# Kernel tuning notes

Measured on AMD Instinct MI355X. Metric: run time of the kernel, lower is better.

The kernel has to match this reference:

```python
import jax, jax.numpy as jnp
import numpy as np

NPOINT = 1024
BRANCHES = [(0.4, 32), (0.8, 64)]  # (radius, nsample)
SPECS = [[67, 64, 64, 128], [67, 64, 128, 256]]  # mlp specs after use_xyz (+3)
EPS = 1e-5


def setup_inputs() -> dict:
    key = jax.random.key(0)
    ks = jax.random.split(key, 16)
    B, N, C = 8, 8192, 64
    inp = {
        "xyz": jax.random.normal(ks[0], (B, N, 3), jnp.float32),
        "features": jax.random.normal(ks[1], (B, C, N), jnp.float32),
    }
    ki = 2
    for bi, spec in enumerate(SPECS):
        for li in range(3):
            o, i = spec[li + 1], spec[li]
            inp[f"w{bi}_{li}"] = jax.random.normal(ks[ki], (o, i), jnp.float32) * (1.0 / np.sqrt(i)); ki += 1
            inp[f"g{bi}_{li}"] = jnp.ones((o,), jnp.float32)
            inp[f"b{bi}_{li}"] = jnp.zeros((o,), jnp.float32)
    return inp


def fps(pts, npoint):
    # pts: [B, N+1, 3] (mean point prepended); sequential farthest point sampling
    B, N1, _ = pts.shape

    def step(carry, _):
        dist, far = carry
        idx3 = jnp.broadcast_to(far[:, None, None], (B, 1, 3))
        centroid = jnp.take_along_axis(pts, idx3, axis=1)  # [B,1,3]
        d = jnp.sum((pts - centroid) ** 2, axis=-1)        # [B,N+1]
        dist = jnp.minimum(dist, d)
        far2 = jnp.argmax(dist, axis=-1)
        return (dist, far2), centroid[:, 0, :]

    dist0 = jnp.full((B, N1), 1e10, jnp.float32)
    far0 = jnp.zeros((B,), jnp.int32)
    _, locs = jax.lax.scan(step, (dist0, far0), None, length=npoint)
    return jnp.transpose(locs, (1, 0, 2))  # [B, npoint, 3]


def ball_query(xyz, new_xyz, radius, nsample):
    # first <=nsample indices with dist^2 < radius^2, padded with first valid (0 if none)
    B, N, _ = xyz.shape
    d2 = jnp.sum((new_xyz[:, :, None, :] - xyz[:, None, :, :]) ** 2, axis=-1)  # [B,S,N]
    score = jnp.where(d2 < radius * radius, jnp.arange(N, dtype=jnp.int32), N)
    vals, _ = jax.lax.top_k(-score, nsample)  # smallest scores = earliest valid indices
    idx = -vals                               # [B,S,nsample], N marks invalid
    first = idx[..., :1]
    first = jnp.where(first < N, first, 0)
    return jnp.where(idx < N, idx, first)


def _forward(xyz, features, params):
    mean = jnp.mean(xyz, axis=1, keepdims=True)
    pts = jnp.concatenate([mean, xyz], axis=1)          # prepend mean point
    new_xyz = jax.lax.stop_gradient(fps(pts, NPOINT))   # [B,npoint,3] (torch no_grad)
    outs = []
    for (radius, nsample), layers in zip(BRANCHES, params):
        idx = ball_query(xyz, new_xyz, radius, nsample)           # [B,S,K]
        gxyz = jax.vmap(lambda p, i: p[i])(xyz, idx)              # [B,S,K,3]
        rel = jnp.transpose(gxyz - new_xyz[:, :, None, :], (0, 3, 1, 2))  # [B,3,S,K]
        gfeat = jax.vmap(lambda f, i: f[:, i])(features, idx)     # [B,C,S,K]
        x = jnp.concatenate([rel, gfeat], axis=1)                 # [B,3+C,S,K]
        for W, g, b in layers:  # Conv2d 1x1 (no bias) + BatchNorm (train stats) + ReLU
            x = jnp.einsum('oi,bisk->bosk', W, x)
            m = jnp.mean(x, axis=(0, 2, 3), keepdims=True)
            v = jnp.var(x, axis=(0, 2, 3), keepdims=True)
            x = (x - m) / jnp.sqrt(v + EPS) * g[None, :, None, None] + b[None, :, None, None]
            x = jax.nn.relu(x)
        outs.append(jnp.max(x, axis=3))                           # [B,Cout,S]
    return new_xyz, jnp.concatenate(outs, axis=1)


def reference(xyz, features,
              w0_0, g0_0, b0_0, w0_1, g0_1, b0_1, w0_2, g0_2, b0_2,
              w1_0, g1_0, b1_0, w1_1, g1_1, b1_1, w1_2, g1_2, b1_2):
    params = [
        [(w0_0, g0_0, b0_0), (w0_1, g0_1, b0_1), (w0_2, g0_2, b0_2)],
        [(w1_0, g1_0, b1_0), (w1_1, g1_1, b1_1), (w1_2, g1_2, b1_2)],
    ]
    return _forward(xyz, features, params)
```

## Files before the change

kernel.cpp:

```cpp
#include <hip/hip_runtime.h>
#include <hip/hip_bf16.h>
#include <cstdint>


typedef __attribute__((ext_vector_type(8))) short short8;
typedef __attribute__((ext_vector_type(4))) float f32x4;

__device__ __forceinline__ float bf2f(unsigned short u) {
    return __uint_as_float(((unsigned)u) << 16);
}
__device__ __forceinline__ unsigned short f2bf(float f) {
    unsigned u = __float_as_uint(f);
    return (unsigned short)((u + 0x7fffu + ((u >> 16) & 1u)) >> 16);
}

__device__ __forceinline__ float wave_red_max_f32(float v) {
#define DPPSTEP(ctrl)                                                                  \
    {                                                                                  \
        int _t = __builtin_amdgcn_update_dpp((int)0xFF800000, __float_as_int(v), ctrl, \
                                             0xf, 0xf, false);                         \
        v = fmaxf(v, __int_as_float(_t));                                              \
    }
    DPPSTEP(0x111) DPPSTEP(0x112) DPPSTEP(0x114) DPPSTEP(0x118) DPPSTEP(0x142) DPPSTEP(0x143)
#undef DPPSTEP
    return v;
}
__device__ __forceinline__ unsigned wave_red_min_u32(unsigned v) {
#define DPPSTEP(ctrl)                                                                   \
    {                                                                                   \
        unsigned _t = (unsigned)__builtin_amdgcn_update_dpp((int)0xFFFFFFFF, (int)v,    \
                                                            ctrl, 0xf, 0xf, false);     \
        v = v < _t ? v : _t;                                                            \
    }
    DPPSTEP(0x111) DPPSTEP(0x112) DPPSTEP(0x114) DPPSTEP(0x118) DPPSTEP(0x142) DPPSTEP(0x143)
#undef DPPSTEP
    return v;
}

static const size_t OFF_WBF   = 0;
static const size_t OFF_STATS = 262144;
static const size_t STATS_BYTES = 720896;
static const size_t OFF_AFF   = 1048576;
static const size_t OFF_IDX0  = 2097152;
static const size_t OFF_IDX1  = 3145728;
static const size_t OFF_MX    = 5242880;
static const size_t OFF_MN    = 13631488;
static const size_t OFF_Y0    = 22020096;
static const size_t OFF_Y1    = 90177536;
static const size_t OFF_FEATT = 211812352;

__global__ void prep_wbf(const float* __restrict__ w0, const float* __restrict__ w1,
                         const float* __restrict__ w2, const float* __restrict__ w3,
                         const float* __restrict__ w4, const float* __restrict__ w5,
                         unsigned short* __restrict__ wb) {
    int id = blockIdx.x * 256 + threadIdx.x;
    const int psz[6] = {6144, 4096, 8192, 6144, 8192, 32768};
    const int Kp[6] = {96, 64, 64, 96, 64, 128};
    const int Ks[6] = {67, 64, 64, 67, 64, 128};
    const float* wp[6] = {w0, w1, w2, w3, w4, w5};
    int off = 0;
    for (int l = 0; l < 6; ++l) {
        if (id < off + psz[l]) {
            int e = id - off;
            int m = e / Kp[l], k = e - m * Kp[l];
            float v = (k < Ks[l]) ? wp[l][m * Ks[l] + k] : 0.f;
            wb[id] = f2bf(v);
            return;
        }
        off += psz[l];
    }
}

__global__ __launch_bounds__(256) void feat_transpose(const float* __restrict__ xyz,
                                                      const float* __restrict__ feat,
                                                      unsigned short* __restrict__ ft) {
    __shared__ float tile[64][65];
    const int b = blockIdx.y;
    const int j0 = blockIdx.x * 64;
    const int tid = threadIdx.x;
#pragma unroll
    for (int i = 0; i < 16; ++i) {
        int e = i * 256 + tid;
        int c = e >> 6, j = e & 63;
        tile[j][c] = feat[((size_t)b * 64 + c) * 8192 + j0 + j];
    }
    __syncthreads();
#pragma unroll
    for (int i = 0; i < 16; ++i) {
        int e = i * 256 + tid;
        int j = e >> 6, c = e & 63;
        ft[((size_t)(b * 8192 + j0 + j)) * 96 + 3 + c] = f2bf(tile[j][c]);
    }
    if (tid < 64) {
        int j = tid;
        size_t base = ((size_t)(b * 8192 + j0 + j)) * 96;
        const float* xp = xyz + ((size_t)b * 8192 + j0 + j) * 3;
        ft[base + 0] = f2bf(xp[0]);
        ft[base + 1] = f2bf(xp[1]);
        ft[base + 2] = f2bf(xp[2]);
    } else if (tid < 128) {
        int j = tid - 64;
        size_t base = ((size_t)(b * 8192 + j0 + j)) * 96;
        for (int c = 67; c < 96; ++c) ft[base + c] = 0;
    }
}

__global__ __launch_bounds__(512) void fps_kernel(const float* __restrict__ xyz,
                                                  float* __restrict__ newxyz) {
    const int b = blockIdx.x;
    const int t = threadIdx.x;
    const int lane = t & 63, wv = t >> 6;
    const float* xb = xyz + (size_t)b * 8192 * 3;

    __shared__ float ptsx[8200];
    __shared__ float ptsy[8200];
    __shared__ float ptsz[8200];
    __shared__ float ldsM[16][3];
    __shared__ float meanv[3];
    __shared__ alignas(16) unsigned long long sKey[2][8];

    float px[16], py[16], pz[16], d[16];
#pragma unroll
    for (int j = 0; j < 16; ++j) {
        int q = t + 512 * j;
        px[j] = xb[q * 3 + 0];
        py[j] = xb[q * 3 + 1];
        pz[j] = xb[q * 3 + 2];
        d[j] = 1e10f;
        ptsx[q + 1] = px[j];
        ptsy[q + 1] = py[j];
        ptsz[q + 1] = pz[j];
    }
    float sxA = 0.f, syA = 0.f, szA = 0.f;
    float sxB = 0.f, syB = 0.f, szB = 0.f;
    int uA = (t + 1023) & 1023;
    int uB = (t + 511) & 1023;
#pragma unroll
    for (int j = 0; j < 8; ++j) {
        int ia = uA + 1024 * j;
        int ib = uB + 1024 * j;
        sxA += xb[ia * 3 + 0]; syA += xb[ia * 3 + 1]; szA += xb[ia * 3 + 2];
        sxB += xb[ib * 3 + 0]; syB += xb[ib * 3 + 1]; szB += xb[ib * 3 + 2];
    }
#pragma unroll
    for (int off = 32; off; off >>= 1) {
        sxA += __shfl_xor(sxA, off, 64);
        syA += __shfl_xor(syA, off, 64);
        szA += __shfl_xor(szA, off, 64);
        sxB += __shfl_xor(sxB, off, 64);
        syB += __shfl_xor(syB, off, 64);
        szB += __shfl_xor(szB, off, 64);
    }
    if (lane == 0) {
        ldsM[wv][0] = sxA; ldsM[wv][1] = syA; ldsM[wv][2] = szA;
        ldsM[wv + 8][0] = sxB; ldsM[wv + 8][1] = syB; ldsM[wv + 8][2] = szB;
    }
    __syncthreads();
    if (t < 3) {
        float s = 0.f;
        for (int w = 0; w < 16; ++w) s += ldsM[w][t];
        meanv[t] = s * (1.f / 8192.f);
    }
    __syncthreads();
    float cx = meanv[0], cy = meanv[1], cz = meanv[2];
    const float mmx = cx, mmy = cy, mmz = cz;
    float dm = 1e10f;
    if (t == 0) { ptsx[0] = cx; ptsy[0] = cy; ptsz[0] = cz; }
    __syncthreads();

    for (int it = 0; it < 1024; ++it) {
        if (t == 0) {
            float* o = newxyz + ((size_t)b * 1024 + it) * 3;
            o[0] = cx; o[1] = cy; o[2] = cz;
        }
        float vmax = -1e30f;
#pragma unroll
        for (int j = 0; j < 16; ++j) {
            float dx = __fsub_rn(px[j], cx);
            float dy = __fsub_rn(py[j], cy);
            float dz = __fsub_rn(pz[j], cz);
            float dd = __fadd_rn(__fadd_rn(__fmul_rn(dx, dx), __fmul_rn(dy, dy)), __fmul_rn(dz, dz));
            float nd = fminf(d[j], dd);
            d[j] = nd;
            vmax = fmaxf(vmax, nd);
        }
        if (t == 0) {
            float dx = __fsub_rn(mmx, cx);
            float dy = __fsub_rn(mmy, cy);
            float dz = __fsub_rn(mmz, cz);
            float dd = __fadd_rn(__fadd_rn(__fmul_rn(dx, dx), __fmul_rn(dy, dy)), __fmul_rn(dz, dz));
            dm = fminf(dm, dd);
            vmax = fmaxf(vmax, dm);
        }
        float wm = wave_red_max_f32(vmax);
        float bmaxw = __int_as_float(__builtin_amdgcn_readlane(__float_as_int(wm), 63));
        unsigned mi = 0xFFFFFFFFu;
#pragma unroll
        for (int j = 15; j >= 0; --j) mi = (d[j] == bmaxw) ? (unsigned)(t + 512 * j + 1) : mi;
        if (t == 0 && dm == bmaxw) mi = 0u;
        unsigned wmin = wave_red_min_u32(mi);
        unsigned miw = (unsigned)__builtin_amdgcn_readlane((int)wmin, 63);
        int par = it & 1;
        if (lane == 0)
            sKey[par][wv] = ((unsigned long long)__float_as_uint(bmaxw) << 32) |
                            (unsigned long long)(8192u - miw);
        __syncthreads();
        unsigned long long k = sKey[par][0];
#pragma unroll
        for (int i = 1; i < 8; ++i) {
            unsigned long long o = sKey[par][i];
            if (o > k) k = o;
        }
        int far = 8192 - (int)(unsigned)(k & 0xffffffffull);
        cx = ptsx[far];
        cy = ptsy[far];
        cz = ptsz[far];
    }
}

__global__ void ball_query_kernel(const float* __restrict__ xyz, const float* __restrict__ newxyz,
                                  int* __restrict__ idxout, float r2, int K) {
    int wid = (blockIdx.x * blockDim.x + threadIdx.x) >> 6;
    int lane = threadIdx.x & 63;
    int b = wid >> 10;
    const float* q = newxyz + (size_t)wid * 3;
    float qx = q[0], qy = q[1], qz = q[2];
    const float* xb = xyz + (size_t)b * 8192 * 3;
    int* out = idxout + (size_t)wid * K;
    int count = 0;
    int first = 0;
    for (int base = 0; base < 8192 && count < K; base += 64) {
        int j = base + lane;
        float dx = __fsub_rn(xb[j * 3 + 0], qx);
        float dy = __fsub_rn(xb[j * 3 + 1], qy);
        float dz = __fsub_rn(xb[j * 3 + 2], qz);
        float d2 = __fadd_rn(__fadd_rn(__fmul_rn(dx, dx), __fmul_rn(dy, dy)), __fmul_rn(dz, dz));
        bool in = d2 < r2;
        unsigned long long m = __ballot(in);
        if (count == 0 && m) first = base + __ffsll((long long)m) - 1;
        if (in) {
            int pos = count + __popcll(m & ((1ull << lane) - 1ull));
            if (pos < K) out[pos] = j;
        }
        count += __popcll(m);
    }
    if (count < K) {
        int fillv = (count > 0) ? first : 0;
        for (int p = count + lane; p < K; p += 64) out[p] = fillv;
    }
}

template <int Mp, int Kp, int IN_MODE, int OUT_MODE, int KSH>
__global__ __launch_bounds__(256) void gemm_mfma(
    const unsigned short* __restrict__ Wb, const unsigned short* __restrict__ Xin,
    const float* __restrict__ aff, const int* __restrict__ idx,
    const unsigned short* __restrict__ ftp, const float* __restrict__ newxyz,
    unsigned short* __restrict__ Yout, float* __restrict__ MX, float* __restrict__ MN,
    float* __restrict__ statS, float* __restrict__ statQ) {
    constexpr int MT = Mp / 64;
    constexpr int KS = Kp / 32;
    const int tid = threadIdx.x;
    const int w = tid >> 6;
    const int lane = tid & 63;
    const int n = lane & 15;
    const int quad = lane >> 4;
    const int rbase = w * (Mp / 4);
    const long col0 = (long)blockIdx.x * 64;

    short8 a[MT][KS];
#pragma unroll
    for (int mt = 0; mt < MT; ++mt)
#pragma unroll
        for (int ks = 0; ks < KS; ++ks)
            a[mt][ks] = *(const short8*)(Wb + (size_t)(rbase + mt * 16 + n) * Kp + ks * 32 + quad * 8);

    f32x4 acc[MT][4];
#pragma unroll
    for (int mt = 0; mt < MT; ++mt)
#pragma unroll
        for (int nt = 0; nt < 4; ++nt)
#pragma unroll
            for (int r = 0; r < 4; ++r) acc[mt][nt][r] = 0.f;

    long fbase[4];
    float qv0[4], qv1[4], qv2[4];
    if constexpr (IN_MODE == 0) {
        int bb = (int)(col0 >> (KSH + 10));
#pragma unroll
        for (int nt = 0; nt < 4; ++nt) {
            long col = col0 + nt * 16 + n;
            int j = idx[col];
            fbase[nt] = ((long)bb * 8192 + j) * 96;
            long sk = col >> KSH;
            qv0[nt] = newxyz[sk * 3 + 0];
            qv1[nt] = newxyz[sk * 3 + 1];
            qv2[nt] = newxyz[sk * 3 + 2];
        }
    }

#pragma unroll
    for (int ks = 0; ks < KS; ++ks) {
        float sc[8], sh[8];
        if constexpr (IN_MODE == 1) {
#pragma unroll
            for (int e = 0; e < 8; ++e) {
                sc[e] = aff[ks * 32 + quad * 8 + e];
                sh[e] = aff[Kp + ks * 32 + quad * 8 + e];
            }
        }
#pragma unroll
        for (int nt = 0; nt < 4; ++nt) {
            short8 bfr;
            if constexpr (IN_MODE == 0) {
                bfr = *(const short8*)(ftp + fbase[nt] + ks * 32 + quad * 8);
                if (ks == 0 && quad == 0) {
                    bfr[0] = (short)f2bf(bf2f((unsigned short)bfr[0]) - qv0[nt]);
                    bfr[1] = (short)f2bf(bf2f((unsigned short)bfr[1]) - qv1[nt]);
                    bfr[2] = (short)f2bf(bf2f((unsigned short)bfr[2]) - qv2[nt]);
                }
            } else {
                long col = col0 + nt * 16 + n;
                short8 raw = *(const short8*)(Xin + col * Kp + ks * 32 + quad * 8);
#pragma unroll
                for (int e = 0; e < 8; ++e) {
                    float xf = bf2f((unsigned short)raw[e]);
                    xf = fmaxf(fmaf(xf, sc[e], sh[e]), 0.f);
                    bfr[e] = (short)f2bf(xf);
                }
            }
#pragma unroll
            for (int mt = 0; mt < MT; ++mt)
                acc[mt][nt] = __builtin_amdgcn_mfma_f32_16x16x32_bf16(a[mt][ks], bfr, acc[mt][nt], 0, 0, 0);
        }
    }

    const int slot = (int)(blockIdx.x & 127);
#pragma unroll
    for (int mt = 0; mt < MT; ++mt)
#pragma unroll
        for (int r = 0; r < 4; ++r) {
            float s = 0.f, q = 0.f;
#pragma unroll
            for (int nt = 0; nt < 4; ++nt) {
                float v = acc[mt][nt][r];
                s += v;
                q = fmaf(v, v, q);
            }
#pragma unroll
            for (int off = 1; off < 16; off <<= 1) {
                s += __shfl_xor(s, off, 16);
                q += __shfl_xor(q, off, 16);
            }
            if (n == 0) {
                int ch = rbase + mt * 16 + quad * 4 + r;
                atomicAdd(statS + (size_t)ch * 128 + slot, s);
                atomicAdd(statQ + (size_t)ch * 128 + slot, q);
            }
        }

    if constexpr (OUT_MODE == 0) {
#pragma unroll
        for (int mt = 0; mt < MT; ++mt)
#pragma unroll
            for (int nt = 0; nt < 4; ++nt) {
                long col = col0 + nt * 16 + n;
                unsigned p0 = f2bf(acc[mt][nt][0]) | ((unsigned)f2bf(acc[mt][nt][1]) << 16);
                unsigned p1 = f2bf(acc[mt][nt][2]) | ((unsigned)f2bf(acc[mt][nt][3]) << 16);
                uint2 st; st.x = p0; st.y = p1;
                *(uint2*)(Yout + col * Mp + rbase + mt * 16 + quad * 4) = st;
            }
    } else {
#pragma unroll
        for (int mt = 0; mt < MT; ++mt)
#pragma unroll
            for (int r = 0; r < 4; ++r) {
                if constexpr (KSH == 6) {
                    float mx = acc[mt][0][r], mn = acc[mt][0][r];
#pragma unroll
                    for (int nt = 1; nt < 4; ++nt) {
                        mx = fmaxf(mx, acc[mt][nt][r]);
                        mn = fminf(mn, acc[mt][nt][r]);
                    }
#pragma unroll
                    for (int off = 1; off < 16; off <<= 1) {
                        mx = fmaxf(mx, __shfl_xor(mx, off, 16));
                        mn = fminf(mn, __shfl_xor(mn, off, 16));
                    }
                    if (n == 0) {
                        int ch = rbase + mt * 16 + quad * 4 + r;
                        long g = col0 >> 6;
                        MX[(long)ch * 8192 + g] = mx;
                        MN[(long)ch * 8192 + g] = mn;
                    }
                } else {
#pragma unroll
                    for (int gh = 0; gh < 2; ++gh) {
                        float mx = fmaxf(acc[mt][2 * gh][r], acc[mt][2 * gh + 1][r]);
                        float mn = fminf(acc[mt][2 * gh][r], acc[mt][2 * gh + 1][r]);
#pragma unroll
                        for (int off = 1; off < 16; off <<= 1) {
                            mx = fmaxf(mx, __shfl_xor(mx, off, 16));
                            mn = fminf(mn, __shfl_xor(mn, off, 16));
                        }
                        if (n == 0) {
                            int ch = rbase + mt * 16 + quad * 4 + r;
                            long g = (col0 >> 5) + gh;
                            MX[(long)ch * 8192 + g] = mx;
                            MN[(long)ch * 8192 + g] = mn;
                        }
                    }
                }
            }
    }
}

__global__ void finalize_kernel(const float* __restrict__ sS, const float* __restrict__ sQ,
                                const float* __restrict__ g, const float* __restrict__ b,
                                float* __restrict__ aff, int C, float invCount) {
    int c = threadIdx.x + blockIdx.x * blockDim.x;
    if (c >= C) return;
    float s = 0.f, q = 0.f;
    for (int k = 0; k < 128; ++k) { s += sS[c * 128 + k]; q += sQ[c * 128 + k]; }
    float mean = s * invCount;
    float var = fmaxf(q * invCount - mean * mean, 0.f);
    float sc = g[c] / sqrtf(var + 1e-5f);
    float sh = b[c] - mean * sc;
    aff[c] = sc;
    aff[C + c] = sh;
}

__global__ void final_out_kernel(const float* __restrict__ MX, const float* __restrict__ MN,
                                 const float* __restrict__ aff, float* __restrict__ out1,
                                 int Cout, int cOff) {
    long i = (long)blockIdx.x * 256 + threadIdx.x;
    int c = (int)(i >> 13);
    int gidx = (int)(i & 8191);
    int b = gidx >> 10, s = gidx & 1023;
    float sc = aff[c], sh = aff[Cout + c];
    float v = fmaxf(fmaxf(sc * MX[i] + sh, sc * MN[i] + sh), 0.f);
    out1[((long)b * 384 + cOff + c) * 1024 + s] = v;
}

extern "C" void kernel_launch(void* const* d_in, const int* in_sizes, int n_in,
                              void* d_out, int out_size, void* d_ws, size_t ws_size,
                              hipStream_t stream) {
    const float* xyz = (const float*)d_in[0];
    const float* feat = (const float*)d_in[1];
    const float *W[6], *G[6], *Bi[6];
    for (int l = 0; l < 6; ++l) {
        W[l] = (const float*)d_in[2 + l * 3];
        G[l] = (const float*)d_in[3 + l * 3];
        Bi[l] = (const float*)d_in[4 + l * 3];
    }
    char* ws = (char*)d_ws;
    float* out0 = (float*)d_out;
    float* out1 = (float*)d_out + 24576;

    unsigned short* wb = (unsigned short*)(ws + OFF_WBF);
    float* stats = (float*)(ws + OFF_STATS);
    float* affine = (float*)(ws + OFF_AFF);
    int* idx0 = (int*)(ws + OFF_IDX0);
    int* idx1 = (int*)(ws + OFF_IDX1);
    float* mx = (float*)(ws + OFF_MX);
    float* mn = (float*)(ws + OFF_MN);
    unsigned short* y0 = (unsigned short*)(ws + OFF_Y0);
    unsigned short* y1 = (unsigned short*)(ws + OFF_Y1);
    unsigned short* ftp = (unsigned short*)(ws + OFF_FEATT);

    hipMemsetAsync(stats, 0, STATS_BYTES, stream);
    prep_wbf<<<256, 256, 0, stream>>>(W[0], W[1], W[2], W[3], W[4], W[5], wb);
    feat_transpose<<<dim3(128, 8), 256, 0, stream>>>(xyz, feat, ftp);
    fps_kernel<<<8, 512, 0, stream>>>(xyz, out0);

    const int wOff[6] = {0, 6144, 10240, 18432, 24576, 32768};
    int stOff[6], afOff[6];
    {
        const int Cs[6] = {64, 64, 128, 64, 128, 256};
        int so = 0, ao = 0;
        for (int l = 0; l < 6; ++l) {
            stOff[l] = so; so += Cs[l] * 256;
            afOff[l] = ao; ao += Cs[l] * 2;
        }
    }

    for (int br = 0; br < 2; ++br) {
        const int K = br ? 64 : 32;
        const float radius = br ? 0.8f : 0.4f;
        const long NCOL = 8L * 1024 * K;
        int* idx = br ? idx1 : idx0;
        const int l0 = br * 3, l1 = br * 3 + 1, l2 = br * 3 + 2;
        const int M2 = br ? 256 : 128;
        const float invCount = 1.f / (float)NCOL;
        const int nblk = (int)(NCOL / 64);

        ball_query_kernel<<<2048, 256, 0, stream>>>(xyz, out0, idx, radius * radius, K);

        if (br == 0) {
            gemm_mfma<64, 96, 0, 0, 5><<<nblk, 256, 0, stream>>>(
                wb + wOff[l0], nullptr, nullptr, idx, ftp, out0, y0, nullptr, nullptr,
                stats + stOff[l0], stats + stOff[l0] + 64 * 128);
            finalize_kernel<<<1, 256, 0, stream>>>(stats + stOff[l0], stats + stOff[l0] + 64 * 128,
                                                   G[l0], Bi[l0], affine + afOff[l0], 64, invCount);
            gemm_mfma<64, 64, 1, 0, 5><<<nblk, 256, 0, stream>>>(
                wb + wOff[l1], y0, affine + afOff[l0], nullptr, nullptr, nullptr, y1, nullptr,
                nullptr, stats + stOff[l1], stats + stOff[l1] + 64 * 128);
            finalize_kernel<<<1, 256, 0, stream>>>(stats + stOff[l1], stats + stOff[l1] + 64 * 128,
                                                   G[l1], Bi[l1], affine + afOff[l1], 64, invCount);
            gemm_mfma<128, 64, 1, 1, 5><<<nblk, 256, 0, stream>>>(
                wb + wOff[l2], y1, affine + afOff[l1], nullptr, nullptr, nullptr, nullptr, mx, mn,
                stats + stOff[l2], stats + stOff[l2] + 128 * 128);
            finalize_kernel<<<1, 256, 0, stream>>>(stats + stOff[l2], stats + stOff[l2] + 128 * 128,
                                                   G[l2], Bi[l2], affine + afOff[l2], 128, invCount);
        } else {
            gemm_mfma<64, 96, 0, 0, 6><<<nblk, 256, 0, stream>>>(
                wb + wOff[l0], nullptr, nullptr, idx, ftp, out0, y0, nullptr, nullptr,
                stats + stOff[l0], stats + stOff[l0] + 64 * 128);
            finalize_kernel<<<1, 256, 0, stream>>>(stats + stOff[l0], stats + stOff[l0] + 64 * 128,
                                                   G[l0], Bi[l0], affine + afOff[l0], 64, invCount);
            gemm_mfma<128, 64, 1, 0, 6><<<nblk, 256, 0, stream>>>(
                wb + wOff[l1], y0, affine + afOff[l0], nullptr, nullptr, nullptr, y1, nullptr,
                nullptr, stats + stOff[l1], stats + stOff[l1] + 128 * 128);
            finalize_kernel<<<1, 256, 0, stream>>>(stats + stOff[l1], stats + stOff[l1] + 128 * 128,
                                                   G[l1], Bi[l1], affine + afOff[l1], 128, invCount);
            gemm_mfma<256, 128, 1, 1, 6><<<nblk, 256, 0, stream>>>(
                wb + wOff[l2], y1, affine + afOff[l1], nullptr, nullptr, nullptr, nullptr, mx, mn,
                stats + stOff[l2], stats + stOff[l2] + 256 * 128);
            finalize_kernel<<<1, 256, 0, stream>>>(stats + stOff[l2], stats + stOff[l2] + 256 * 128,
                                                   G[l2], Bi[l2], affine + afOff[l2], 256, invCount);
        }

        final_out_kernel<<<(M2 * 8192) / 256, 256, 0, stream>>>(mx, mn, affine + afOff[l2], out1,
                                                                M2, br ? 128 : 0);
    }
}
```

Measured before the change: 1.792 ms.

## Fuse FPS, feature transpose and weight prep into one launch with packed FPS math

```diff
diff --git a/kernel.cpp b/kernel.cpp
--- a/kernel.cpp
+++ b/kernel.cpp
@@ -5,6 +5,7 @@
 
 typedef __attribute__((ext_vector_type(8))) short short8;
 typedef __attribute__((ext_vector_type(4))) float f32x4;
+typedef __attribute__((ext_vector_type(2))) float f32x2;
 
 __device__ __forceinline__ float bf2f(unsigned short u) {
     return __uint_as_float(((unsigned)u) << 16);
@@ -36,6 +37,10 @@
 #undef DPPSTEP
     return v;
 }
+__device__ __forceinline__ unsigned long long u64max(unsigned long long a, unsigned long long b) {
+    return a > b ? a : b;
+}
+__device__ __forceinline__ unsigned u32min(unsigned a, unsigned b) { return a < b ? a : b; }
 
 static const size_t OFF_WBF   = 0;
 static const size_t OFF_STATS = 262144;
@@ -49,87 +54,92 @@
 static const size_t OFF_Y1    = 90177536;
 static const size_t OFF_FEATT = 211812352;
 
-__global__ void prep_wbf(const float* __restrict__ w0, const float* __restrict__ w1,
-                         const float* __restrict__ w2, const float* __restrict__ w3,
-                         const float* __restrict__ w4, const float* __restrict__ w5,
-                         unsigned short* __restrict__ wb) {
-    int id = blockIdx.x * 256 + threadIdx.x;
-    const int psz[6] = {6144, 4096, 8192, 6144, 8192, 32768};
-    const int Kp[6] = {96, 64, 64, 96, 64, 128};
-    const int Ks[6] = {67, 64, 64, 67, 64, 128};
-    const float* wp[6] = {w0, w1, w2, w3, w4, w5};
-    int off = 0;
-    for (int l = 0; l < 6; ++l) {
-        if (id < off + psz[l]) {
-            int e = id - off;
-            int m = e / Kp[l], k = e - m * Kp[l];
-            float v = (k < Ks[l]) ? wp[l][m * Ks[l] + k] : 0.f;
-            wb[id] = f2bf(v);
-            return;
-        }
-        off += psz[l];
-    }
-}
-
-__global__ __launch_bounds__(256) void feat_transpose(const float* __restrict__ xyz,
-                                                      const float* __restrict__ feat,
-                                                      unsigned short* __restrict__ ft) {
-    __shared__ float tile[64][65];
-    const int b = blockIdx.y;
-    const int j0 = blockIdx.x * 64;
+__global__ __launch_bounds__(512) void fused_pre(
+    const float* __restrict__ xyz, const float* __restrict__ feat,
+    float* __restrict__ newxyz, unsigned short* __restrict__ ft,
+    const float* __restrict__ w0, const float* __restrict__ w1, const float* __restrict__ w2,
+    const float* __restrict__ w3, const float* __restrict__ w4, const float* __restrict__ w5,
+    unsigned short* __restrict__ wb) {
+    __shared__ union alignas(16) SM {
+        struct {
+            float ptsx[8200], ptsy[8200], ptsz[8200];
+            float ldsM[16][3];
+            float meanv[3];
+            unsigned long long sKey[2][8];
+        } f;
+        float tile[64][65];
+    } sm;
     const int tid = threadIdx.x;
-#pragma unroll
-    for (int i = 0; i < 16; ++i) {
-        int e = i * 256 + tid;
-        int c = e >> 6, j = e & 63;
-        tile[j][c] = feat[((size_t)b * 64 + c) * 8192 + j0 + j];
-    }
-    __syncthreads();
-#pragma unroll
-    for (int i = 0; i < 16; ++i) {
-        int e = i * 256 + tid;
-        int j = e >> 6, c = e & 63;
-        ft[((size_t)(b * 8192 + j0 + j)) * 96 + 3 + c] = f2bf(tile[j][c]);
-    }
-    if (tid < 64) {
-        int j = tid;
-        size_t base = ((size_t)(b * 8192 + j0 + j)) * 96;
-        const float* xp = xyz + ((size_t)b * 8192 + j0 + j) * 3;
-        ft[base + 0] = f2bf(xp[0]);
-        ft[base + 1] = f2bf(xp[1]);
-        ft[base + 2] = f2bf(xp[2]);
-    } else if (tid < 128) {
-        int j = tid - 64;
-        size_t base = ((size_t)(b * 8192 + j0 + j)) * 96;
-        for (int c = 67; c < 96; ++c) ft[base + c] = 0;
-    }
-}
-
-__global__ __launch_bounds__(512) void fps_kernel(const float* __restrict__ xyz,
-                                                  float* __restrict__ newxyz) {
+
+    if (blockIdx.x >= 1032) {
+        int id = (int)(blockIdx.x - 1032) * 512 + tid;
+        const int psz[6] = {6144, 4096, 8192, 6144, 8192, 32768};
+        const int Kp[6] = {96, 64, 64, 96, 64, 128};
+        const int Ks[6] = {67, 64, 64, 67, 64, 128};
+        const float* wp[6] = {w0, w1, w2, w3, w4, w5};
+        int off = 0;
+        for (int l = 0; l < 6; ++l) {
+            if (id < off + psz[l]) {
+                int e = id - off;
+                int m = e / Kp[l], k = e - m * Kp[l];
+                float v = (k < Ks[l]) ? wp[l][m * Ks[l] + k] : 0.f;
+                wb[id] = f2bf(v);
+                return;
+            }
+            off += psz[l];
+        }
+        return;
+    }
+
+    if (blockIdx.x >= 8) {
+        int tb = (int)blockIdx.x - 8;
+        int b = tb >> 7;
+        int j0 = (tb & 127) * 64;
+#pragma unroll
+        for (int i = 0; i < 8; ++i) {
+            int e = i * 512 + tid;
+            int c = e >> 6, j = e & 63;
+            sm.tile[j][c] = feat[((size_t)b * 64 + c) * 8192 + j0 + j];
+        }
+        __syncthreads();
+#pragma unroll
+        for (int i = 0; i < 8; ++i) {
+            int e = i * 512 + tid;
+            int j = e >> 6, c = e & 63;
+            ft[((size_t)(b * 8192 + j0 + j)) * 96 + 3 + c] = f2bf(sm.tile[j][c]);
+        }
+        if (tid < 64) {
+            int j = tid;
+            size_t base = ((size_t)(b * 8192 + j0 + j)) * 96;
+            const float* xp = xyz + ((size_t)b * 8192 + j0 + j) * 3;
+            ft[base + 0] = f2bf(xp[0]);
+            ft[base + 1] = f2bf(xp[1]);
+            ft[base + 2] = f2bf(xp[2]);
+        } else if (tid < 128) {
+            int j = tid - 64;
+            size_t base = ((size_t)(b * 8192 + j0 + j)) * 96;
+            for (int c = 67; c < 96; ++c) ft[base + c] = 0;
+        }
+        return;
+    }
+
     const int b = blockIdx.x;
-    const int t = threadIdx.x;
+    const int t = tid;
     const int lane = t & 63, wv = t >> 6;
     const float* xb = xyz + (size_t)b * 8192 * 3;
 
-    __shared__ float ptsx[8200];
-    __shared__ float ptsy[8200];
-    __shared__ float ptsz[8200];
-    __shared__ float ldsM[16][3];
-    __shared__ float meanv[3];
-    __shared__ alignas(16) unsigned long long sKey[2][8];
-
-    float px[16], py[16], pz[16], d[16];
-#pragma unroll
-    for (int j = 0; j < 16; ++j) {
-        int q = t + 512 * j;
-        px[j] = xb[q * 3 + 0];
-        py[j] = xb[q * 3 + 1];
-        pz[j] = xb[q * 3 + 2];
-        d[j] = 1e10f;
-        ptsx[q + 1] = px[j];
-        ptsy[q + 1] = py[j];
-        ptsz[q + 1] = pz[j];
+    f32x2 px[8], py[8], pz[8], d[8];
+#pragma unroll
+    for (int k = 0; k < 8; ++k) {
+        int q0 = t + 512 * (2 * k);
+        int q1 = t + 512 * (2 * k + 1);
+        px[k].x = xb[q0 * 3 + 0]; px[k].y = xb[q1 * 3 + 0];
+        py[k].x = xb[q0 * 3 + 1]; py[k].y = xb[q1 * 3 + 1];
+        pz[k].x = xb[q0 * 3 + 2]; pz[k].y = xb[q1 * 3 + 2];
+        d[k].x = 1e10f; d[k].y = 1e10f;
+        sm.f.ptsx[q0 + 1] = px[k].x; sm.f.ptsx[q1 + 1] = px[k].y;
+        sm.f.ptsy[q0 + 1] = py[k].x; sm.f.ptsy[q1 + 1] = py[k].y;
+        sm.f.ptsz[q0 + 1] = pz[k].x; sm.f.ptsz[q1 + 1] = pz[k].y;
     }
     float sxA = 0.f, syA = 0.f, szA = 0.f;
     float sxB = 0.f, syB = 0.f, szB = 0.f;
@@ -152,20 +162,20 @@
         szB += __shfl_xor(szB, off, 64);
     }
     if (lane == 0) {
-        ldsM[wv][0] = sxA; ldsM[wv][1] = syA; ldsM[wv][2] = szA;
-        ldsM[wv + 8][0] = sxB; ldsM[wv + 8][1] = syB; ldsM[wv + 8][2] = szB;
+        sm.f.ldsM[wv][0] = sxA; sm.f.ldsM[wv][1] = syA; sm.f.ldsM[wv][2] = szA;
+        sm.f.ldsM[wv + 8][0] = sxB; sm.f.ldsM[wv + 8][1] = syB; sm.f.ldsM[wv + 8][2] = szB;
     }
     __syncthreads();
     if (t < 3) {
         float s = 0.f;
-        for (int w = 0; w < 16; ++w) s += ldsM[w][t];
-        meanv[t] = s * (1.f / 8192.f);
+        for (int w = 0; w < 16; ++w) s += sm.f.ldsM[w][t];
+        sm.f.meanv[t] = s * (1.f / 8192.f);
     }
     __syncthreads();
-    float cx = meanv[0], cy = meanv[1], cz = meanv[2];
+    float cx = sm.f.meanv[0], cy = sm.f.meanv[1], cz = sm.f.meanv[2];
     const float mmx = cx, mmy = cy, mmz = cz;
     float dm = 1e10f;
-    if (t == 0) { ptsx[0] = cx; ptsy[0] = cy; ptsz[0] = cz; }
+    if (t == 0) { sm.f.ptsx[0] = cx; sm.f.ptsy[0] = cy; sm.f.ptsz[0] = cz; }
     __syncthreads();
 
     for (int it = 0; it < 1024; ++it) {
@@ -173,17 +183,23 @@
             float* o = newxyz + ((size_t)b * 1024 + it) * 3;
             o[0] = cx; o[1] = cy; o[2] = cz;
         }
-        float vmax = -1e30f;
-#pragma unroll
-        for (int j = 0; j < 16; ++j) {
-            float dx = __fsub_rn(px[j], cx);
-            float dy = __fsub_rn(py[j], cy);
-            float dz = __fsub_rn(pz[j], cz);
-            float dd = __fadd_rn(__fadd_rn(__fmul_rn(dx, dx), __fmul_rn(dy, dy)), __fmul_rn(dz, dz));
-            float nd = fminf(d[j], dd);
-            d[j] = nd;
-            vmax = fmaxf(vmax, nd);
-        }
+        f32x2 c0, c1, c2, vm2;
+        c0.x = cx; c0.y = cx; c1.x = cy; c1.y = cy; c2.x = cz; c2.y = cz;
+        vm2.x = -1e30f; vm2.y = -1e30f;
+        {
+#pragma clang fp contract(off)
+#pragma unroll
+            for (int k = 0; k < 8; ++k) {
+                f32x2 dx = px[k] - c0;
+                f32x2 dy = py[k] - c1;
+                f32x2 dz = pz[k] - c2;
+                f32x2 dd = (dx * dx + dy * dy) + dz * dz;
+                f32x2 nd = __builtin_elementwise_min(d[k], dd);
+                d[k] = nd;
+                vm2 = __builtin_elementwise_max(vm2, nd);
+            }
+        }
+        float vmax = fmaxf(vm2.x, vm2.y);
         if (t == 0) {
             float dx = __fsub_rn(mmx, cx);
             float dy = __fsub_rn(mmy, cy);
@@ -194,27 +210,34 @@
         }
         float wm = wave_red_max_f32(vmax);
         float bmaxw = __int_as_float(__builtin_amdgcn_readlane(__float_as_int(wm), 63));
-        unsigned mi = 0xFFFFFFFFu;
-#pragma unroll
-        for (int j = 15; j >= 0; --j) mi = (d[j] == bmaxw) ? (unsigned)(t + 512 * j + 1) : mi;
+        unsigned m2[8];
+#pragma unroll
+        for (int k = 0; k < 8; ++k) {
+            unsigned i0 = (d[k].x == bmaxw) ? (unsigned)(t + 512 * (2 * k) + 1) : 0xFFFFFFFFu;
+            unsigned i1 = (d[k].y == bmaxw) ? (unsigned)(t + 512 * (2 * k + 1) + 1) : 0xFFFFFFFFu;
+            m2[k] = u32min(i0, i1);
+        }
+        unsigned n0 = u32min(m2[0], m2[1]), n1 = u32min(m2[2], m2[3]);
+        unsigned n2 = u32min(m2[4], m2[5]), n3 = u32min(m2[6], m2[7]);
+        unsigned mi = u32min(u32min(n0, n1), u32min(n2, n3));
         if (t == 0 && dm == bmaxw) mi = 0u;
         unsigned wmin = wave_red_min_u32(mi);
         unsigned miw = (unsigned)__builtin_amdgcn_readlane((int)wmin, 63);
         int par = it & 1;
         if (lane == 0)
-            sKey[par][wv] = ((unsigned long long)__float_as_uint(bmaxw) << 32) |
-                            (unsigned long long)(8192u - miw);
+            sm.f.sKey[par][wv] = ((unsigned long long)__float_as_uint(bmaxw) << 32) |
+                                 (unsigned long long)(8192u - miw);
         __syncthreads();
-        unsigned long long k = sKey[par][0];
-#pragma unroll
-        for (int i = 1; i < 8; ++i) {
-            unsigned long long o = sKey[par][i];
-            if (o > k) k = o;
-        }
-        int far = 8192 - (int)(unsigned)(k & 0xffffffffull);
-        cx = ptsx[far];
-        cy = ptsy[far];
-        cz = ptsz[far];
+        unsigned long long ka[8];
+#pragma unroll
+        for (int i = 0; i < 8; ++i) ka[i] = sm.f.sKey[par][i];
+        unsigned long long p0 = u64max(ka[0], ka[1]), p1 = u64max(ka[2], ka[3]);
+        unsigned long long p2 = u64max(ka[4], ka[5]), p3 = u64max(ka[6], ka[7]);
+        unsigned long long kk = u64max(u64max(p0, p1), u64max(p2, p3));
+        int far = 8192 - (int)(unsigned)(kk & 0xffffffffull);
+        cx = sm.f.ptsx[far];
+        cy = sm.f.ptsy[far];
+        cz = sm.f.ptsz[far];
     }
 }
 
@@ -468,9 +491,8 @@
     unsigned short* ftp = (unsigned short*)(ws + OFF_FEATT);
 
     hipMemsetAsync(stats, 0, STATS_BYTES, stream);
-    prep_wbf<<<256, 256, 0, stream>>>(W[0], W[1], W[2], W[3], W[4], W[5], wb);
-    feat_transpose<<<dim3(128, 8), 256, 0, stream>>>(xyz, feat, ftp);
-    fps_kernel<<<8, 512, 0, stream>>>(xyz, out0);
+    fused_pre<<<1160, 512, 0, stream>>>(xyz, feat, out0, ftp, W[0], W[1], W[2], W[3], W[4],
+                                        W[5], wb);
 
     const int wOff[6] = {0, 6144, 10240, 18432, 24576, 32768};
     int stOff[6], afOff[6];
```

After: 1.773 ms. About the same (-1.1%).
